# Kernel tuning notes

Measured on AMD Instinct MI355X. Metric: run time of the kernel, lower is better.

## Reference

```python
import jax, jax.numpy as jnp
import numpy as np

D = 256        # in_dim == out_dim for both node types
NH = 8         # n_heads
DH = D // NH   # d_over_h = 32
NA = 50000     # nodes of type 'a'
NB = 20000     # nodes of type 'b'
E = 100000     # edges per edge type
MAX_LEN = 27759
LN_EPS = 1e-5


def _rte_table():
    # Fixed (non-trainable) sinusoidal table from RelativeTemporalEncoding
    pos = np.arange(MAX_LEN, dtype=np.float32)[:, None]
    div = np.exp(np.arange(0, D, 2, dtype=np.float32) * (-np.log(10000.0) / D))
    tab = np.zeros((MAX_LEN, D), dtype=np.float32)
    tab[:, 0::2] = np.sin(pos * div) / np.sqrt(D)
    tab[:, 1::2] = np.cos(pos * div) / np.sqrt(D)
    return jnp.asarray(tab)


def setup_inputs() -> dict:
    key = jax.random.key(0)
    ks = jax.random.split(key, 24)
    s = 1.0 / np.sqrt(D)
    sh = 1.0 / np.sqrt(DH)
    inp = {
        "Ha": jax.random.normal(ks[0], (NA, D), jnp.float32),
        "Hb": jax.random.normal(ks[1], (NB, D), jnp.float32),
        "rte_emb": _rte_table(),
        # stacked per-node-type weights, index 0 -> 'a', 1 -> 'b'; torch Linear layout [out, in]
        "Wq": jax.random.normal(ks[2], (2, D, D), jnp.float32) * s,
        "Wk": jax.random.normal(ks[3], (2, D, D), jnp.float32) * s,
        "Wm": jax.random.normal(ks[4], (2, D, D), jnp.float32) * s,
        "Wa": jax.random.normal(ks[5], (2, D, D), jnp.float32) * s,
        "rteW": jax.random.normal(ks[6], (2, D, D), jnp.float32) * s,
        "rteb": jnp.zeros((2, D), jnp.float32),
        "ln_g": jnp.ones((2, D), jnp.float32),
        "ln_b": jnp.zeros((2, D), jnp.float32),
        "res_alpha": jnp.ones((2,), jnp.float32),
        # stacked per-edge-type params, index 0 -> e1 (a->a), 1 -> e2 (b->a), 2 -> e3 (a->b)
        "Watt": jax.random.normal(ks[7], (3, DH, DH), jnp.float32) * sh,
        "Wmsg": jax.random.normal(ks[8], (3, DH, DH), jnp.float32) * sh,
        "prior": jnp.ones((3,), jnp.float32),
        "src1": jax.random.randint(ks[9], (E,), 0, NA, jnp.int32),
        "dst1": jax.random.randint(ks[10], (E,), 0, NA, jnp.int32),
        "t1": jax.random.randint(ks[11], (E,), 1, MAX_LEN, jnp.int32),
        "src2": jax.random.randint(ks[12], (E,), 0, NB, jnp.int32),
        "dst2": jax.random.randint(ks[13], (E,), 0, NA, jnp.int32),
        "t2": jax.random.randint(ks[14], (E,), 1, MAX_LEN, jnp.int32),
        "src3": jax.random.randint(ks[15], (E,), 0, NA, jnp.int32),
        "dst3": jax.random.randint(ks[16], (E,), 0, NB, jnp.int32),
        "t3": jax.random.randint(ks[17], (E,), 1, MAX_LEN, jnp.int32),
    }
    return inp


def _edge_agg(Hs, Hd, src, dst, t, Wk_s, Wm_s, Wq_t, rW, rb, Wa_e, Wm_e, pr, rte_emb, n_dst):
    """Per-edge-type attention + segment softmax + weighted scatter-sum."""
    ne = src.shape[0]
    # RTE on gathered source features: h_src + Linear(emb[27759 - time])
    hs = Hs[src] + rte_emb[MAX_LEN - t] @ rW.T + rb            # [E, D]
    K = (hs @ Wk_s.T).reshape(ne, NH, DH)                       # [E, H, DH]
    Q = (Hd[dst] @ Wq_t.T).reshape(ne, NH, DH)                  # [E, H, DH]
    att = jnp.einsum('ehd,df,ehf->eh', K, Wa_e, Q) * pr / np.sqrt(DH).astype(np.float32)
    msg = jnp.einsum('ehd,df->ehf', (hs @ Wm_s.T).reshape(ne, NH, DH), Wm_e)
    # segment softmax over destination nodes (DGL mailbox softmax)
    amax = jax.lax.stop_gradient(jax.ops.segment_max(att, dst, num_segments=n_dst))
    ex = jnp.exp(att - amax[dst])
    den = jax.ops.segment_sum(ex, dst, num_segments=n_dst)
    w = ex / den[dst]                                           # [E, H]
    agg = jax.ops.segment_sum(w[..., None] * msg, dst, num_segments=n_dst)  # [N, H, DH]
    cnt = jax.ops.segment_sum(jnp.ones((ne,), jnp.float32), dst, num_segments=n_dst)
    return agg, (cnt > 0).astype(jnp.float32)


def _update(agg, Hx, Wa_n, g, b, ra):
    x = jax.nn.elu(agg.reshape(agg.shape[0], -1)) @ Wa_n.T
    alpha = jax.nn.sigmoid(ra)
    u = alpha * x + (1.0 - alpha) * Hx
    mu = jnp.mean(u, axis=-1, keepdims=True)
    var = jnp.var(u, axis=-1, keepdims=True)
    return (u - mu) / jnp.sqrt(var + LN_EPS) * g + b


def reference(Ha, Hb, rte_emb, Wq, Wk, Wm, Wa, rteW, rteb, ln_g, ln_b, res_alpha,
              Watt, Wmsg, prior, src1, dst1, t1, src2, dst2, t2, src3, dst3, t3):
    # e1: a -> a ; e2: b -> a ; e3: a -> b
    agg1, h1 = _edge_agg(Ha, Ha, src1, dst1, t1, Wk[0], Wm[0], Wq[0], rteW[0], rteb[0], Watt[0], Wmsg[0], prior[0], rte_emb, NA)
    agg2, h2 = _edge_agg(Hb, Ha, src2, dst2, t2, Wk[1], Wm[1], Wq[0], rteW[1], rteb[1], Watt[1], Wmsg[1], prior[1], rte_emb, NA)
    agg3, h3 = _edge_agg(Ha, Hb, src3, dst3, t3, Wk[0], Wm[0], Wq[1], rteW[0], rteb[0], Watt[2], Wmsg[2], prior[2], rte_emb, NB)
    # cross_reducer='mean': average over edge types that delivered messages
    agg_a = (agg1 + agg2) / jnp.maximum(h1 + h2, 1.0)[:, None, None]
    agg_b = agg3 / jnp.maximum(h3, 1.0)[:, None, None]
    out_a = _update(agg_a, Ha, Wa[0], ln_g[0], ln_b[0], res_alpha[0])
    out_b = _update(agg_b, Hb, Wa[1], ln_g[1], ln_b[1], res_alpha[1])
    return (out_a, out_b)
```

## Files before the change

### kernel.cpp

```cpp
#include <hip/hip_runtime.h>
#include <hip/hip_bf16.h>
#include <math.h>

typedef __hip_bfloat16 bf16;
typedef __attribute__((ext_vector_type(8))) short bf16x8v;
typedef __attribute__((ext_vector_type(4))) float f32x4;


__device__ __forceinline__ float eluf(float x) { return x > 0.f ? x : (__expf(x) - 1.f); }
__device__ __forceinline__ float b2f(unsigned short u) { return __uint_as_float((unsigned)u << 16); }
__device__ __forceinline__ unsigned short f2b(float f) {
    unsigned u = __float_as_uint(f);
    return (unsigned short)((u + 0x7fffu + ((u >> 16) & 1u)) >> 16);
}
__device__ __forceinline__ void unpack8(uint4 u, float* o) {
    o[0] = __uint_as_float(u.x << 16); o[1] = __uint_as_float(u.x & 0xffff0000u);
    o[2] = __uint_as_float(u.y << 16); o[3] = __uint_as_float(u.y & 0xffff0000u);
    o[4] = __uint_as_float(u.z << 16); o[5] = __uint_as_float(u.z & 0xffff0000u);
    o[6] = __uint_as_float(u.w << 16); o[7] = __uint_as_float(u.w & 0xffff0000u);
}
__device__ __forceinline__ void unpack4(ushort4 u, float* o) {
    o[0] = b2f(u.x); o[1] = b2f(u.y); o[2] = b2f(u.z); o[3] = b2f(u.w);
}

#define ASYNC_LDS16(g, l) \
    __builtin_amdgcn_global_load_lds((const __attribute__((address_space(1))) void*)(g), \
                                     (__attribute__((address_space(3))) void*)(l), 16, 0, 0)

__global__ void conv_multi_kernel(
    const float* s0, bf16* o0, int n0, const float* s1, bf16* o1, int n1,
    const float* s2, bf16* o2, int n2, const float* s3, bf16* o3, int n3,
    const float* s4, bf16* o4, int n4, const float* s5, bf16* o5, int n5,
    int* z0, int nz0, int* z1, int nz1)
{
    if (blockIdx.y == 6) {
        for (int i = blockIdx.x * 256 + threadIdx.x; i < nz0; i += gridDim.x * 256) z0[i] = 0;
        if (blockIdx.x == 0 && threadIdx.x < (unsigned)nz1) z1[threadIdx.x] = 0;
        return;
    }
    const float* sp; bf16* op; int n8;
    switch (blockIdx.y) {
        case 0: sp = s0; op = o0; n8 = n0; break;
        case 1: sp = s1; op = o1; n8 = n1; break;
        case 2: sp = s2; op = o2; n8 = n2; break;
        case 3: sp = s3; op = o3; n8 = n3; break;
        case 4: sp = s4; op = o4; n8 = n4; break;
        default: sp = s5; op = o5; n8 = n5; break;
    }
    for (int i = blockIdx.x * 256 + threadIdx.x; i < n8; i += gridDim.x * 256) {
        const float4* p = (const float4*)(sp + (size_t)i * 8);
        float4 a = p[0], b = p[1];
        uint4 u;
        u.x = (unsigned)f2b(a.x) | ((unsigned)f2b(a.y) << 16);
        u.y = (unsigned)f2b(a.z) | ((unsigned)f2b(a.w) << 16);
        u.z = (unsigned)f2b(b.x) | ((unsigned)f2b(b.y) << 16);
        u.w = (unsigned)f2b(b.z) | ((unsigned)f2b(b.w) << 16);
        *(uint4*)(op + (size_t)i * 8) = u;
    }
}

__global__ void fold6_kernel(const float* __restrict__ Watt, const float* __restrict__ Wmsg,
                             const float* __restrict__ prior,
                             const float* __restrict__ Wq, const float* __restrict__ Wm,
                             bf16* __restrict__ WcatA, bf16* __restrict__ WcatB,
                             float* __restrict__ Wmx1f, float* __restrict__ Wmx2f,
                             float* __restrict__ Wmx3f)
{
    const int g = blockIdx.x >> 8;
    const int i = blockIdx.x & 255;
    const int j = threadIdx.x;
    const int h = i >> 5, r = i & 31;
    const float* A; const float* W; float sc = 1.f; int tr = 0;
    bf16* ob; float* of = nullptr;
    const float isq = 0.17677669529663687f;
    switch (g) {
        case 0: A = Watt;        sc = prior[0] * isq; W = Wq;         ob = WcatA;                       break;
        case 1: A = Watt + 1024; sc = prior[1] * isq; W = Wq;         ob = WcatA + (size_t)256 * 256;   break;
        case 2: A = Watt + 2048; sc = prior[2] * isq; W = Wq + 65536; ob = WcatB;                       break;
        case 3: A = Wmsg;        tr = 1; W = Wm;         ob = WcatA + (size_t)768 * 256;  of = Wmx1f;   break;
        case 4: A = Wmsg + 1024; tr = 1; W = Wm + 65536; ob = WcatB + (size_t)512 * 256;  of = Wmx2f;   break;
        default:A = Wmsg + 2048; tr = 1; W = Wm;         ob = WcatA + (size_t)1024 * 256; of = Wmx3f;   break;
    }
    __shared__ float arow[32];
    if (j < 32) arow[j] = (tr ? A[j * 32 + r] : A[r * 32 + j]) * sc;
    __syncthreads();
    float acc = 0.f;
    for (int k = 0; k < 32; ++k) acc += arow[k] * W[(size_t)(h * 32 + k) * 256 + j];
    ((unsigned short*)ob)[(size_t)i * 256 + j] = f2b(acc);
    if (of) of[(size_t)i * 256 + j] = acc;
}

__global__ void combine5_kernel(const float* __restrict__ Wk,
                                const float* __restrict__ Wmx1f, const float* __restrict__ Wmx2f,
                                const float* __restrict__ Wmx3f,
                                const float* __restrict__ rteW, const float* __restrict__ rteb,
                                bf16* __restrict__ WcatR, float* __restrict__ bcatR)
{
    const int g = blockIdx.x >> 8;
    const int i = blockIdx.x & 255;
    const int j = threadIdx.x;
    const float* Wp; const float* rW; const float* rb; int op;
    switch (g) {
        case 0: Wp = Wk;         rW = rteW;         rb = rteb;       op = 0; break;
        case 1: Wp = Wk + 65536; rW = rteW + 65536; rb = rteb + 256; op = 2; break;
        case 2: Wp = Wmx1f;      rW = rteW;         rb = rteb;       op = 1; break;
        case 3: Wp = Wmx2f;      rW = rteW + 65536; rb = rteb + 256; op = 3; break;
        default:Wp = Wmx3f;      rW = rteW;         rb = rteb;       op = 4; break;
    }
    __shared__ float wrow[256];
    wrow[j] = Wp[i * 256 + j];
    __syncthreads();
    float acc = 0.f;
    for (int k = 0; k < 256; ++k) acc += wrow[k] * rW[k * 256 + j];
    ((unsigned short*)WcatR)[(size_t)(op * 256 + i) * 256 + j] = f2b(acc);
    if (j == 0) {
        float b = 0.f;
        for (int k = 0; k < 256; ++k) b += wrow[k] * rb[k];
        bcatR[op * 256 + i] = b;
    }
}

__device__ __forceinline__ void gemm_body(
    const bf16* __restrict__ A, const bf16* __restrict__ Wcat,
    const float* __restrict__ bcat,
    bf16* C0, bf16* C1, bf16* C2, bf16* C3, bf16* C4,
    int wideMask, int M, int bx, int by, char* As, char* Bs)
{
    const int tid = threadIdx.x;
    const int wid = tid >> 6, lane = tid & 63;
    const size_t row0 = (size_t)bx * 128;
    const int gcol0 = by * 128;
    const int cb = by >> 1;
    const int lcol0 = (by & 1) * 128;
    bf16* Csel = (cb == 0) ? C0 : (cb == 1) ? C1 : (cb == 2) ? C2 : (cb == 3) ? C3 : C4;
    const size_t cstride = ((wideMask >> cb) & 1) ? 512 : 256;
    const int wr = wid >> 1, wc = wid & 1;

    f32x4 zero = {0.f, 0.f, 0.f, 0.f};
    f32x4 acc[4][4];
#pragma unroll
    for (int m = 0; m < 4; ++m)
#pragma unroll
        for (int n = 0; n < 4; ++n) acc[m][n] = zero;

    const int sr = wid * 32 + (lane >> 3);
    const int scc = (lane & 7) << 4;
    const char* Ab = (const char*)A;
    const char* Wb = (const char*)Wcat;

    for (int k0 = 0; k0 < 512; k0 += 128) {
#pragma unroll
        for (int i = 0; i < 4; ++i) {
            const int r = sr + i * 8;
            const int csw = scc ^ ((r & 7) << 4);
            const int ldso = wid * 4096 + i * 1024;
            ASYNC_LDS16(Ab + (row0 + r) * 512 + k0 + csw, As + ldso);
            ASYNC_LDS16(Wb + (size_t)(gcol0 + r) * 512 + k0 + csw, Bs + ldso);
        }
        __syncthreads();
#pragma unroll
        for (int kk = 0; kk < 2; ++kk) {
            bf16x8v a[4], b[4];
            const int cbase = kk * 64 + ((lane >> 4) << 4);
#pragma unroll
            for (int m = 0; m < 4; ++m) {
                const int r = wr * 64 + m * 16 + (lane & 15);
                a[m] = *(const bf16x8v*)(As + r * 128 + (cbase ^ ((r & 7) << 4)));
            }
#pragma unroll
            for (int n = 0; n < 4; ++n) {
                const int r = wc * 64 + n * 16 + (lane & 15);
                b[n] = *(const bf16x8v*)(Bs + r * 128 + (cbase ^ ((r & 7) << 4)));
            }
#pragma unroll
            for (int m = 0; m < 4; ++m)
#pragma unroll
                for (int n = 0; n < 4; ++n)
                    acc[m][n] = __builtin_amdgcn_mfma_f32_16x16x32_bf16(a[m], b[n], acc[m][n], 0, 0, 0);
        }
        __syncthreads();
    }
    const int orow = (lane >> 4) << 2;
    const int ocol = lane & 15;
    float bv[4];
#pragma unroll
    for (int n = 0; n < 4; ++n)
        bv[n] = bcat ? bcat[gcol0 + wc * 64 + n * 16 + ocol] : 0.f;
    unsigned short* Cp = (unsigned short*)Csel;
#pragma unroll
    for (int m = 0; m < 4; ++m) {
#pragma unroll
        for (int j = 0; j < 4; ++j) {
            const size_t row = row0 + wr * 64 + m * 16 + orow + j;
            if ((int)row >= M) continue;
#pragma unroll
            for (int n = 0; n < 4; ++n) {
                const int col = lcol0 + wc * 64 + n * 16 + ocol;
                Cp[row * cstride + col] = f2b(acc[m][n][j] + bv[n]);
            }
        }
    }
}

__global__ __launch_bounds__(256) void gemm3_kernel(
    const bf16* A0, const bf16* W0, const float* bc0,
    bf16* o00, bf16* o01, bf16* o02, bf16* o03, bf16* o04, int mask0, int M0,
    const bf16* A1, const bf16* W1,
    bf16* o10, bf16* o11, bf16* o12, bf16* o13, bf16* o14, int mask1, int M1,
    const bf16* A2, const bf16* W2,
    bf16* o20, bf16* o21, bf16* o22, int mask2, int M2,
    int b0, int b1)
{
    __shared__ __align__(16) char As[16384];
    __shared__ __align__(16) char Bs[16384];
    const int bid = blockIdx.x;
    if (bid < b0) {
        gemm_body(A0, W0, bc0, o00, o01, o02, o03, o04, mask0, M0,
                  bid / 10, bid % 10, As, Bs);
    } else if (bid < b1) {
        const int lid = bid - b0;
        gemm_body(A1, W1, nullptr, o10, o11, o12, o13, o14, mask1, M1,
                  lid / 10, lid % 10, As, Bs);
    } else {
        const int lid = bid - b1;
        gemm_body(A2, W2, nullptr, o20, o21, o22, o22, o22, mask2, M2,
                  lid / 6, lid % 6, As, Bs);
    }
}

__global__ __launch_bounds__(512) void ugemm_ln_kernel(
    const bf16* __restrict__ AG, const bf16* __restrict__ Wp,
    const bf16* __restrict__ Hbf, const float* __restrict__ g,
    const float* __restrict__ b, const float* __restrict__ ra,
    float* __restrict__ out, int M)
{
    __shared__ __align__(16) char As[16384];
    __shared__ __align__(16) char Bs[32768];
    __shared__ float red[128][8];
    const int tid = threadIdx.x;
    const int wid = tid >> 6, lane = tid & 63;
    const int wr = wid >> 2, wc = wid & 3;
    const size_t row0 = (size_t)blockIdx.x * 128;

    f32x4 zero = {0.f, 0.f, 0.f, 0.f};
    f32x4 acc[4][4];
#pragma unroll
    for (int m = 0; m < 4; ++m)
#pragma unroll
        for (int n = 0; n < 4; ++n) acc[m][n] = zero;

    const char* Ab = (const char*)AG;
    const char* Wb = (const char*)Wp;
    for (int k0 = 0; k0 < 512; k0 += 128) {
#pragma unroll
        for (int i = 0; i < 2; ++i) {
            const int r = wid * 16 + i * 8 + (lane >> 3);
            const int csw = ((lane & 7) << 4) ^ ((r & 7) << 4);
            ASYNC_LDS16(Ab + (row0 + r) * 512 + k0 + csw, As + (wid * 16 + i * 8) * 128);
        }
#pragma unroll
        for (int i = 0; i < 4; ++i) {
            const int r = wid * 32 + i * 8 + (lane >> 3);
            const int csw = ((lane & 7) << 4) ^ ((r & 7) << 4);
            ASYNC_LDS16(Wb + (size_t)r * 512 + k0 + csw, Bs + (wid * 32 + i * 8) * 128);
        }
        __syncthreads();
#pragma unroll
        for (int kk = 0; kk < 2; ++kk) {
            bf16x8v a[4], bv[4];
            const int cbase = kk * 64 + ((lane >> 4) << 4);
#pragma unroll
            for (int m = 0; m < 4; ++m) {
                const int r = wr * 64 + m * 16 + (lane & 15);
                a[m] = *(const bf16x8v*)(As + r * 128 + (cbase ^ ((r & 7) << 4)));
            }
#pragma unroll
            for (int n = 0; n < 4; ++n) {
                const int r = wc * 64 + n * 16 + (lane & 15);
                bv[n] = *(const bf16x8v*)(Bs + r * 128 + (cbase ^ ((r & 7) << 4)));
            }
#pragma unroll
            for (int m = 0; m < 4; ++m)
#pragma unroll
                for (int n = 0; n < 4; ++n)
                    acc[m][n] = __builtin_amdgcn_mfma_f32_16x16x32_bf16(a[m], bv[n], acc[m][n], 0, 0, 0);
        }
        __syncthreads();
    }
    const float alpha = 1.f / (1.f + __expf(-ra[0]));
    const float beta = 1.f - alpha;
    const int orow = (lane >> 4) << 2;
    const int ocol = lane & 15;
    float gv[4], bb[4];
#pragma unroll
    for (int n = 0; n < 4; ++n) {
        gv[n] = g[wc * 64 + n * 16 + ocol];
        bb[n] = b[wc * 64 + n * 16 + ocol];
    }
    const unsigned short* Hp = (const unsigned short*)Hbf;
#pragma unroll
    for (int m = 0; m < 4; ++m) {
#pragma unroll
        for (int j = 0; j < 4; ++j) {
            const int rl = wr * 64 + m * 16 + orow + j;
            const size_t grow = row0 + rl;
            float s = 0.f, s2 = 0.f;
#pragma unroll
            for (int n = 0; n < 4; ++n) {
                const int col = wc * 64 + n * 16 + ocol;
                float hv = ((int)grow < M) ? b2f(Hp[grow * 256 + col]) : 0.f;
                float u = alpha * acc[m][n][j] + beta * hv;
                acc[m][n][j] = u;
                s += u; s2 += u * u;
            }
            s += __shfl_xor(s, 1); s2 += __shfl_xor(s2, 1);
            s += __shfl_xor(s, 2); s2 += __shfl_xor(s2, 2);
            s += __shfl_xor(s, 4); s2 += __shfl_xor(s2, 4);
            s += __shfl_xor(s, 8); s2 += __shfl_xor(s2, 8);
            if (ocol == 0) { red[rl][wc] = s; red[rl][4 + wc] = s2; }
        }
    }
    __syncthreads();
#pragma unroll
    for (int m = 0; m < 4; ++m) {
#pragma unroll
        for (int j = 0; j < 4; ++j) {
            const int rl = wr * 64 + m * 16 + orow + j;
            const size_t grow = row0 + rl;
            if ((int)grow >= M) continue;
            float S = red[rl][0] + red[rl][1] + red[rl][2] + red[rl][3];
            float S2 = red[rl][4] + red[rl][5] + red[rl][6] + red[rl][7];
            const float mu = S * 0.00390625f;
            const float var = S2 * 0.00390625f - mu * mu;
            const float inv = rsqrtf(var + 1e-5f);
#pragma unroll
            for (int n = 0; n < 4; ++n) {
                const int col = wc * 64 + n * 16 + ocol;
                out[grow * 256 + col] = (acc[m][n][j] - mu) * inv * gv[n] + bb[n];
            }
        }
    }
}

__global__ void hist3_kernel(const int* __restrict__ d1, const int* __restrict__ d2,
                             const int* __restrict__ d3, int* __restrict__ c1,
                             int* __restrict__ c2, int* __restrict__ c3,
                             int E1, int E2, int E3)
{
    int i = blockIdx.x * 256 + threadIdx.x;
    if (i < E1) atomicAdd(&c1[d1[i]], 1);
    else if (i < E1 + E2) atomicAdd(&c2[d2[i - E1]], 1);
    else if (i < E1 + E2 + E3) atomicAdd(&c3[d3[i - E1 - E2]], 1);
}
__global__ void alloc3b_kernel(const int* __restrict__ cnt, int* __restrict__ start,
                               int* __restrict__ cursor, int* __restrict__ gtot,
                               int NA, int NB)
{
    const int slot = blockIdx.y;
    const int base = (slot == 0) ? 0 : (slot == 1) ? NA : 2 * NA;
    const int len = (slot == 2) ? NB : NA;
    int i = blockIdx.x * 256 + threadIdx.x;
    if (i >= len) return;
    int* gp = gtot + slot;
    int idx = base + i;
    int s = atomicAdd(gp, cnt[idx]);
    start[idx] = s; cursor[idx] = s;
}
__global__ void scatter3_kernel(const int* __restrict__ d1, const int* __restrict__ d2,
                                const int* __restrict__ d3, int* __restrict__ cur1,
                                int* __restrict__ cur2, int* __restrict__ cur3,
                                int* __restrict__ el1, int* __restrict__ el2,
                                int* __restrict__ el3, int E1, int E2, int E3)
{
    int i = blockIdx.x * 256 + threadIdx.x;
    if (i < E1) { int p = atomicAdd(&cur1[d1[i]], 1); el1[p] = i; }
    else if (i < E1 + E2) { int e = i - E1; int p = atomicAdd(&cur2[d2[e]], 1); el2[p] = e; }
    else if (i < E1 + E2 + E3) { int e = i - E1 - E2; int p = atomicAdd(&cur3[d3[e]], 1); el3[p] = e; }
}

__device__ __forceinline__ void epass16(
    const bf16* __restrict__ KM, const bf16* __restrict__ RKM,
    const int* __restrict__ srcv, const int* __restrict__ tv, const int* __restrict__ el,
    int beg, int num, const float q[8], int ml, int lane, int srcl,
    float s[8], float& denOut)
{
    float den = 0.f;
    for (int c0 = 0; c0 < num; c0 += 64) {
        int nc = num - c0; if (nc > 64) nc = 64;
        int sx_l = 0, tt_l = 0;
        if (lane < nc) { int e = el[beg + c0 + lane]; sx_l = srcv[e]; tt_l = ml - tv[e]; }
        int sx = __shfl(sx_l, 0), tt = __shfl(tt_l, 0);
        uint4 km = *(const uint4*)(KM + (size_t)sx * 512 + lane * 8);
        uint4 rm = *(const uint4*)(RKM + (size_t)tt * 512 + lane * 8);
        for (int i = 0; i < nc; ++i) {
            uint4 kmn = km, rmn = rm;
            if (i + 1 < nc) {
                int sxn = __shfl(sx_l, i + 1), ttn = __shfl(tt_l, i + 1);
                kmn = *(const uint4*)(KM + (size_t)sxn * 512 + lane * 8);
                rmn = *(const uint4*)(RKM + (size_t)ttn * 512 + lane * 8);
            }
            float a[8], b[8];
            unpack8(km, a); unpack8(rm, b);
#pragma unroll
            for (int x = 0; x < 8; ++x) a[x] += b[x];
            float p = a[0] * q[0] + a[1] * q[1] + a[2] * q[2] + a[3] * q[3]
                    + a[4] * q[4] + a[5] * q[5] + a[6] * q[6] + a[7] * q[7];
            p += __shfl_xor(p, 1); p += __shfl_xor(p, 2);
            float ex = __expf(p);
            float exb = __shfl(ex, srcl);
            den += exb;
#pragma unroll
            for (int x = 0; x < 8; ++x) s[x] += exb * a[x];
            km = kmn; rm = rmn;
        }
    }
    denOut = den;
}

__device__ __forceinline__ void epass8(
    const bf16* __restrict__ Kh, const bf16* __restrict__ RKh,
    const bf16* __restrict__ Mt, const bf16* __restrict__ RMt,
    const int* __restrict__ srcv, const int* __restrict__ tv, const int* __restrict__ el,
    int beg, int num, const float q[4], int ml, int lane,
    float s[4], float& denOut)
{
    float den = 0.f;
    for (int c0 = 0; c0 < num; c0 += 64) {
        int nc = num - c0; if (nc > 64) nc = 64;
        int sx_l = 0, tt_l = 0;
        if (lane < nc) { int e = el[beg + c0 + lane]; sx_l = srcv[e]; tt_l = ml - tv[e]; }
        int sx = __shfl(sx_l, 0), tt = __shfl(tt_l, 0);
        ushort4 kv = *(const ushort4*)(Kh + (size_t)sx * 512 + lane * 4);
        ushort4 rv = *(const ushort4*)(RKh + (size_t)tt * 512 + lane * 4);
        ushort4 mv = *(const ushort4*)(Mt + (size_t)sx * 256 + lane * 4);
        ushort4 uv = *(const ushort4*)(RMt + (size_t)tt * 256 + lane * 4);
        for (int i = 0; i < nc; ++i) {
            ushort4 kn = kv, rn = rv, mn = mv, un = uv;
            if (i + 1 < nc) {
                int sxn = __shfl(sx_l, i + 1), ttn = __shfl(tt_l, i + 1);
                kn = *(const ushort4*)(Kh + (size_t)sxn * 512 + lane * 4);
                rn = *(const ushort4*)(RKh + (size_t)ttn * 512 + lane * 4);
                mn = *(const ushort4*)(Mt + (size_t)sxn * 256 + lane * 4);
                un = *(const ushort4*)(RMt + (size_t)ttn * 256 + lane * 4);
            }
            float a[4], b[4], m[4], r[4];
            unpack4(kv, a); unpack4(rv, b); unpack4(mv, m); unpack4(uv, r);
            float p = (a[0] + b[0]) * q[0] + (a[1] + b[1]) * q[1]
                    + (a[2] + b[2]) * q[2] + (a[3] + b[3]) * q[3];
            p += __shfl_xor(p, 1); p += __shfl_xor(p, 2); p += __shfl_xor(p, 4);
            float ex = __expf(p);
            den += ex;
#pragma unroll
            for (int x = 0; x < 4; ++x) s[x] += ex * (m[x] + r[x]);
            kv = kn; rv = rn; mv = mn; uv = un;
        }
    }
    denOut = den;
}

__global__ __launch_bounds__(256) void edge_fused_kernel(
    const bf16* __restrict__ Qa1, const bf16* __restrict__ Qa2,
    const bf16* __restrict__ KMa1, const bf16* __restrict__ RKM1,
    const int* __restrict__ src1, const int* __restrict__ t1,
    const int* __restrict__ start1, const int* __restrict__ cnt1, const int* __restrict__ el1,
    const bf16* __restrict__ KMb, const bf16* __restrict__ RKM2,
    const int* __restrict__ src2, const int* __restrict__ t2,
    const int* __restrict__ start2, const int* __restrict__ cnt2, const int* __restrict__ el2,
    bf16* __restrict__ AGa, int NA,
    const bf16* __restrict__ Qb3, const bf16* __restrict__ Ma3, const bf16* __restrict__ RM3p,
    const int* __restrict__ src3, const int* __restrict__ t3,
    const int* __restrict__ start3, const int* __restrict__ cnt3, const int* __restrict__ el3,
    bf16* __restrict__ AGb, int NB, int ml, int nablk)
{
    const int wid = threadIdx.x >> 6, lane = threadIdx.x & 63;
    if ((int)blockIdx.x < nablk) {
        const int n = blockIdx.x * 4 + wid;
        if (n >= NA) return;
        float q1[8], q2[8];
        unpack8(*(const uint4*)(Qa1 + (size_t)n * 256 + (lane & 31) * 8), q1);
        unpack8(*(const uint4*)(Qa2 + (size_t)n * 256 + (lane & 31) * 8), q2);
        const int srcl = (lane < 32) ? lane : (((lane - 32) >> 2) << 2);
        const int num1 = cnt1[n], num2 = cnt2[n];
        float sf[8] = {0.f, 0.f, 0.f, 0.f, 0.f, 0.f, 0.f, 0.f};
        float s[8], den;
        if (num1 > 0) {
#pragma unroll
            for (int x = 0; x < 8; ++x) s[x] = 0.f;
            epass16(KMa1, RKM1, src1, t1, el1, start1[n], num1, q1, ml, lane, srcl, s, den);
            float invd = 1.f / den;
#pragma unroll
            for (int x = 0; x < 8; ++x) sf[x] += s[x] * invd;
        }
        if (num2 > 0) {
#pragma unroll
            for (int x = 0; x < 8; ++x) s[x] = 0.f;
            epass16(KMb, RKM2, src2, t2, el2, start2[n], num2, q2, ml, lane, srcl, s, den);
            float invd = 1.f / den;
#pragma unroll
            for (int x = 0; x < 8; ++x) sf[x] += s[x] * invd;
        }
        float dv = 1.f / fmaxf((float)((num1 > 0) + (num2 > 0)), 1.f);
        if (lane >= 32) {
            uint4 o;
            o.x = (unsigned)f2b(eluf(sf[0] * dv)) | ((unsigned)f2b(eluf(sf[1] * dv)) << 16);
            o.y = (unsigned)f2b(eluf(sf[2] * dv)) | ((unsigned)f2b(eluf(sf[3] * dv)) << 16);
            o.z = (unsigned)f2b(eluf(sf[4] * dv)) | ((unsigned)f2b(eluf(sf[5] * dv)) << 16);
            o.w = (unsigned)f2b(eluf(sf[6] * dv)) | ((unsigned)f2b(eluf(sf[7] * dv)) << 16);
            *(uint4*)((unsigned short*)AGa + (size_t)n * 256 + (lane - 32) * 8) = o;
        }
    } else {
        const int n = ((int)blockIdx.x - nablk) * 4 + wid;
        if (n >= NB) return;
        float q3[4];
        unpack4(*(const ushort4*)(Qb3 + (size_t)n * 256 + lane * 4), q3);
        const int num3 = cnt3[n];
        float s[4] = {0.f, 0.f, 0.f, 0.f};
        float den = 1.f;
        if (num3 > 0) {
            epass8(KMa1, RKM1, Ma3, RM3p, src3, t3, el3, start3[n], num3, q3, ml, lane, s, den);
            float invd = 1.f / den;
#pragma unroll
            for (int x = 0; x < 4; ++x) s[x] *= invd;
        }
        ushort4 o;
        o.x = f2b(eluf(s[0])); o.y = f2b(eluf(s[1]));
        o.z = f2b(eluf(s[2])); o.w = f2b(eluf(s[3]));
        *(ushort4*)((unsigned short*)AGb + (size_t)n * 256 + lane * 4) = o;
    }
}

extern "C" void kernel_launch(void* const* d_in, const int* in_sizes, int n_in,
                              void* d_out, int out_size, void* d_ws, size_t ws_size,
                              hipStream_t stream)
{
    const float* Ha   = (const float*)d_in[0];
    const float* Hb   = (const float*)d_in[1];
    const float* rte  = (const float*)d_in[2];
    const float* Wq   = (const float*)d_in[3];
    const float* Wk   = (const float*)d_in[4];
    const float* Wm   = (const float*)d_in[5];
    const float* Wa   = (const float*)d_in[6];
    const float* rteW = (const float*)d_in[7];
    const float* rteb = (const float*)d_in[8];
    const float* ln_g = (const float*)d_in[9];
    const float* ln_b = (const float*)d_in[10];
    const float* ra   = (const float*)d_in[11];
    const float* Watt = (const float*)d_in[12];
    const float* Wmsg = (const float*)d_in[13];
    const float* prior= (const float*)d_in[14];
    const int* src1 = (const int*)d_in[15];
    const int* dst1 = (const int*)d_in[16];
    const int* t1   = (const int*)d_in[17];
    const int* src2 = (const int*)d_in[18];
    const int* dst2 = (const int*)d_in[19];
    const int* t2   = (const int*)d_in[20];
    const int* src3 = (const int*)d_in[21];
    const int* dst3 = (const int*)d_in[22];
    const int* t3   = (const int*)d_in[23];

    const int NA = in_sizes[0] / 256;
    const int NB = in_sizes[1] / 256;
    const int ML = in_sizes[2] / 256;
    const int E1 = in_sizes[15];
    const int E2 = in_sizes[18];
    const int E3 = in_sizes[21];
    const int NAp = (NA + 127) & ~127;
    const int NBp = (NB + 127) & ~127;
    const int MLp = (ML + 127) & ~127;

    char* w = (char*)d_ws;
    size_t off = 0;
    auto alloc = [&](size_t bytes) -> void* {
        void* p = w + off;
        off += (bytes + 511) & ~(size_t)511;
        return p;
    };
    bf16* WcatA = (bf16*)alloc((size_t)1280 * 256 * 2);
    bf16* WcatB = (bf16*)alloc((size_t)768 * 256 * 2);
    bf16* WcatR = (bf16*)alloc((size_t)1280 * 256 * 2);
    float* bcatR = (float*)alloc(1280 * 4);
    bf16* Wa_bf = (bf16*)alloc(131072 * 2);
    float* Wmx1f = (float*)alloc(65536 * 4);
    float* Wmx2f = (float*)alloc(65536 * 4);
    float* Wmx3f = (float*)alloc(65536 * 4);
    bf16* Ha_bf = (bf16*)alloc((size_t)NAp * 512);
    bf16* Hb_bf = (bf16*)alloc((size_t)NBp * 512);
    bf16* rte_bf = (bf16*)alloc((size_t)MLp * 512);
    bf16* Qa1 = (bf16*)alloc((size_t)NAp * 512);
    bf16* Qa2 = (bf16*)alloc((size_t)NAp * 512);
    bf16* KMa1 = (bf16*)alloc((size_t)NAp * 1024);
    bf16* RKM1 = (bf16*)alloc((size_t)MLp * 1024);
    bf16* RKM2 = (bf16*)alloc((size_t)MLp * 1024);
    bf16* RM3p = (bf16*)alloc((size_t)MLp * 512);
    int* cnt = (int*)alloc((size_t)(NA + NA + NB) * 4);
    int* cnt1 = cnt, *cnt2 = cnt + NA, *cnt3 = cnt + 2 * NA;
    int* startb = (int*)alloc((size_t)(NA + NA + NB) * 4);
    int* start1 = startb, *start2 = startb + NA, *start3 = startb + 2 * NA;
    int* curb = (int*)alloc((size_t)(NA + NA + NB) * 4);
    int* cur1 = curb, *cur2 = curb + NA, *cur3 = curb + 2 * NA;
    int* elist1 = (int*)alloc((size_t)E1 * 4);
    int* elist2 = (int*)alloc((size_t)E2 * 4);
    int* elist3 = (int*)alloc((size_t)E3 * 4);
    int* gtot = (int*)alloc(16);
    bf16* Ma3 = (bf16*)d_out;
    bf16* Qb3 = (bf16*)d_out + (size_t)NAp * 256;
    bf16* KMb = (bf16*)d_out + (size_t)NAp * 256 + (size_t)NBp * 256;
    bf16* AGa = Qa1;
    bf16* AGb = Qb3;

    conv_multi_kernel<<<dim3(512, 7), 256, 0, stream>>>(
        Ha, Ha_bf, NA * 32, Hb, Hb_bf, NB * 32, rte, rte_bf, ML * 32,
        Wa, Wa_bf, 16384,
        Wk, WcatA + (size_t)512 * 256, 8192,
        Wk + 65536, WcatB + (size_t)256 * 256, 8192,
        cnt, NA + NA + NB, gtot, 4);
    fold6_kernel<<<1536, 256, 0, stream>>>(Watt, Wmsg, prior, Wq, Wm,
                                           WcatA, WcatB, Wmx1f, Wmx2f, Wmx3f);
    combine5_kernel<<<1280, 256, 0, stream>>>(Wk, Wmx1f, Wmx2f, Wmx3f, rteW, rteb, WcatR, bcatR);

    int Etot = E1 + E2 + E3;
    hist3_kernel<<<dim3((Etot + 255) / 256), 256, 0, stream>>>(dst1, dst2, dst3, cnt1, cnt2, cnt3, E1, E2, E3);
    alloc3b_kernel<<<dim3((NA + 255) / 256, 3), 256, 0, stream>>>(cnt, startb, curb, gtot, NA, NB);
    scatter3_kernel<<<dim3((Etot + 255) / 256), 256, 0, stream>>>(
        dst1, dst2, dst3, cur1, cur2, cur3, elist1, elist2, elist3, E1, E2, E3);

    const int nx0 = MLp / 128, nx1 = NAp / 128, nx2 = NBp / 128;
    const int b0 = nx0 * 10;
    const int b1 = b0 + nx1 * 10;
    const int btot = b1 + nx2 * 6;
    gemm3_kernel<<<dim3(btot), 256, 0, stream>>>(
        rte_bf, WcatR, bcatR, RKM1, RKM1 + 256, RKM2, RKM2 + 256, RM3p, 0xF, ML,
        Ha_bf, WcatA, Qa1, Qa2, KMa1, KMa1 + 256, Ma3, 0xC, NA,
        Hb_bf, WcatB, Qb3, KMb, KMb + 256, 0x6, NB,
        b0, b1);

    const int nablk = (NA + 3) / 4;
    const int nbblk = (NB + 3) / 4;
    edge_fused_kernel<<<dim3(nablk + nbblk), 256, 0, stream>>>(
        Qa1, Qa2, KMa1, RKM1, src1, t1, start1, cnt1, elist1,
        KMb, RKM2, src2, t2, start2, cnt2, elist2,
        AGa, NA,
        Qb3, Ma3, RM3p, src3, t3, start3, cnt3, elist3,
        AGb, NB, ML, nablk);

    float* out = (float*)d_out;
    ugemm_ln_kernel<<<dim3(NBp / 128), 512, 0, stream>>>(
        AGb, Wa_bf + 65536, Hb_bf, ln_g + 256, ln_b + 256, ra + 1,
        out + (size_t)NA * 256, NB);
    ugemm_ln_kernel<<<dim3(NAp / 128), 512, 0, stream>>>(
        AGa, Wa_bf, Ha_bf, ln_g, ln_b, ra, out, NA);
}
```

Measured before the change: 380.7 us.

## Pack src/time into CSR edge list and batch gathers four edges at a time

The scatter kernel now writes (src, ml - t) pairs straight into the CSR edge list, so the edge kernel no longer does a dependent double indirection through el then src/t. The per-edge gather loop is unrolled to issue four edges' K/M row loads before computing, which gives more memory-level parallelism than one-ahead prefetch. First-chunk edge indices are loaded up front for both edge types, and the Q2 unpack is deferred until needed. The cost is doubled edge-list storage and more registers held by the four-way unrolled loads, which may reduce occupancy.

```diff
diff --git a/kernel.cpp b/kernel.cpp
--- a/kernel.cpp
+++ b/kernel.cpp
@@ -367,51 +367,84 @@
     start[idx] = s; cursor[idx] = s;
 }
 __global__ void scatter3_kernel(const int* __restrict__ d1, const int* __restrict__ d2,
-                                const int* __restrict__ d3, int* __restrict__ cur1,
-                                int* __restrict__ cur2, int* __restrict__ cur3,
-                                int* __restrict__ el1, int* __restrict__ el2,
-                                int* __restrict__ el3, int E1, int E2, int E3)
+                                const int* __restrict__ d3,
+                                const int* __restrict__ s1, const int* __restrict__ s2,
+                                const int* __restrict__ s3,
+                                const int* __restrict__ tv1, const int* __restrict__ tv2,
+                                const int* __restrict__ tv3,
+                                int* __restrict__ cur1, int* __restrict__ cur2,
+                                int* __restrict__ cur3,
+                                int2* __restrict__ el1, int2* __restrict__ el2,
+                                int2* __restrict__ el3, int E1, int E2, int E3, int ml)
 {
     int i = blockIdx.x * 256 + threadIdx.x;
-    if (i < E1) { int p = atomicAdd(&cur1[d1[i]], 1); el1[p] = i; }
-    else if (i < E1 + E2) { int e = i - E1; int p = atomicAdd(&cur2[d2[e]], 1); el2[p] = e; }
-    else if (i < E1 + E2 + E3) { int e = i - E1 - E2; int p = atomicAdd(&cur3[d3[e]], 1); el3[p] = e; }
+    if (i < E1) {
+        int p = atomicAdd(&cur1[d1[i]], 1);
+        el1[p] = make_int2(s1[i], ml - tv1[i]);
+    } else if (i < E1 + E2) {
+        int e = i - E1; int p = atomicAdd(&cur2[d2[e]], 1);
+        el2[p] = make_int2(s2[e], ml - tv2[e]);
+    } else if (i < E1 + E2 + E3) {
+        int e = i - E1 - E2; int p = atomicAdd(&cur3[d3[e]], 1);
+        el3[p] = make_int2(s3[e], ml - tv3[e]);
+    }
 }
 
 __device__ __forceinline__ void epass16(
     const bf16* __restrict__ KM, const bf16* __restrict__ RKM,
-    const int* __restrict__ srcv, const int* __restrict__ tv, const int* __restrict__ el,
-    int beg, int num, const float q[8], int ml, int lane, int srcl,
+    const int2* __restrict__ el, int beg, int num,
+    int sx_l, int tt_l,
+    const float q[8], int lane, int srcl,
     float s[8], float& denOut)
 {
     float den = 0.f;
+    const char* KMb = (const char*)KM + lane * 16;
+    const char* RMb = (const char*)RKM + lane * 16;
+    auto edge = [&](uint4 km, uint4 rm) {
+        float a[8], b[8];
+        unpack8(km, a); unpack8(rm, b);
+#pragma unroll
+        for (int x = 0; x < 8; ++x) a[x] += b[x];
+        float p = a[0] * q[0] + a[1] * q[1] + a[2] * q[2] + a[3] * q[3]
+                + a[4] * q[4] + a[5] * q[5] + a[6] * q[6] + a[7] * q[7];
+        p += __shfl_xor(p, 1); p += __shfl_xor(p, 2);
+        float ex = __expf(p);
+        float exb = __shfl(ex, srcl);
+        den += exb;
+#pragma unroll
+        for (int x = 0; x < 8; ++x) s[x] += exb * a[x];
+    };
     for (int c0 = 0; c0 < num; c0 += 64) {
         int nc = num - c0; if (nc > 64) nc = 64;
-        int sx_l = 0, tt_l = 0;
-        if (lane < nc) { int e = el[beg + c0 + lane]; sx_l = srcv[e]; tt_l = ml - tv[e]; }
-        int sx = __shfl(sx_l, 0), tt = __shfl(tt_l, 0);
-        uint4 km = *(const uint4*)(KM + (size_t)sx * 512 + lane * 8);
-        uint4 rm = *(const uint4*)(RKM + (size_t)tt * 512 + lane * 8);
-        for (int i = 0; i < nc; ++i) {
-            uint4 kmn = km, rmn = rm;
-            if (i + 1 < nc) {
-                int sxn = __shfl(sx_l, i + 1), ttn = __shfl(tt_l, i + 1);
-                kmn = *(const uint4*)(KM + (size_t)sxn * 512 + lane * 8);
-                rmn = *(const uint4*)(RKM + (size_t)ttn * 512 + lane * 8);
-            }
-            float a[8], b[8];
-            unpack8(km, a); unpack8(rm, b);
-#pragma unroll
-            for (int x = 0; x < 8; ++x) a[x] += b[x];
-            float p = a[0] * q[0] + a[1] * q[1] + a[2] * q[2] + a[3] * q[3]
-                    + a[4] * q[4] + a[5] * q[5] + a[6] * q[6] + a[7] * q[7];
-            p += __shfl_xor(p, 1); p += __shfl_xor(p, 2);
-            float ex = __expf(p);
-            float exb = __shfl(ex, srcl);
-            den += exb;
-#pragma unroll
-            for (int x = 0; x < 8; ++x) s[x] += exb * a[x];
-            km = kmn; rm = rmn;
+        if (c0 > 0) {
+            sx_l = 0; tt_l = 0;
+            if (lane < nc) { int2 e = el[beg + c0 + lane]; sx_l = e.x; tt_l = e.y; }
+        }
+        for (int i0 = 0; i0 < nc; i0 += 4) {
+            const int rem = nc - i0;
+            const int a0 = __shfl(sx_l, i0),     b0 = __shfl(tt_l, i0);
+            const int a1 = __shfl(sx_l, i0 | 1), b1 = __shfl(tt_l, i0 | 1);
+            const int a2 = __shfl(sx_l, i0 | 2), b2 = __shfl(tt_l, i0 | 2);
+            const int a3 = __shfl(sx_l, i0 | 3), b3 = __shfl(tt_l, i0 | 3);
+            uint4 km0, rm0, km1, rm1, km2, rm2, km3, rm3;
+            km0 = *(const uint4*)(KMb + (size_t)a0 * 1024);
+            rm0 = *(const uint4*)(RMb + (size_t)b0 * 1024);
+            if (rem > 1) {
+                km1 = *(const uint4*)(KMb + (size_t)a1 * 1024);
+                rm1 = *(const uint4*)(RMb + (size_t)b1 * 1024);
+            }
+            if (rem > 2) {
+                km2 = *(const uint4*)(KMb + (size_t)a2 * 1024);
+                rm2 = *(const uint4*)(RMb + (size_t)b2 * 1024);
+            }
+            if (rem > 3) {
+                km3 = *(const uint4*)(KMb + (size_t)a3 * 1024);
+                rm3 = *(const uint4*)(RMb + (size_t)b3 * 1024);
+            }
+            edge(km0, rm0);
+            if (rem > 1) edge(km1, rm1);
+            if (rem > 2) edge(km2, rm2);
+            if (rem > 3) edge(km3, rm3);
         }
     }
     denOut = den;
@@ -420,39 +453,66 @@
 __device__ __forceinline__ void epass8(
     const bf16* __restrict__ Kh, const bf16* __restrict__ RKh,
     const bf16* __restrict__ Mt, const bf16* __restrict__ RMt,
-    const int* __restrict__ srcv, const int* __restrict__ tv, const int* __restrict__ el,
-    int beg, int num, const float q[4], int ml, int lane,
+    const int2* __restrict__ el, int beg, int num,
+    int sx_l, int tt_l,
+    const float q[4], int lane,
     float s[4], float& denOut)
 {
     float den = 0.f;
+    const char* Kb = (const char*)Kh + lane * 8;
+    const char* Rb = (const char*)RKh + lane * 8;
+    const char* Mb = (const char*)Mt + lane * 8;
+    const char* Ub = (const char*)RMt + lane * 8;
+    auto edge = [&](ushort4 kv, ushort4 rv, ushort4 mv, ushort4 uv) {
+        float a[4], b[4], m[4], r[4];
+        unpack4(kv, a); unpack4(rv, b); unpack4(mv, m); unpack4(uv, r);
+        float p = (a[0] + b[0]) * q[0] + (a[1] + b[1]) * q[1]
+                + (a[2] + b[2]) * q[2] + (a[3] + b[3]) * q[3];
+        p += __shfl_xor(p, 1); p += __shfl_xor(p, 2); p += __shfl_xor(p, 4);
+        float ex = __expf(p);
+        den += ex;
+#pragma unroll
+        for (int x = 0; x < 4; ++x) s[x] += ex * (m[x] + r[x]);
+    };
     for (int c0 = 0; c0 < num; c0 += 64) {
         int nc = num - c0; if (nc > 64) nc = 64;
-        int sx_l = 0, tt_l = 0;
-        if (lane < nc) { int e = el[beg + c0 + lane]; sx_l = srcv[e]; tt_l = ml - tv[e]; }
-        int sx = __shfl(sx_l, 0), tt = __shfl(tt_l, 0);
-        ushort4 kv = *(const ushort4*)(Kh + (size_t)sx * 512 + lane * 4);
-        ushort4 rv = *(const ushort4*)(RKh + (size_t)tt * 512 + lane * 4);
-        ushort4 mv = *(const ushort4*)(Mt + (size_t)sx * 256 + lane * 4);
-        ushort4 uv = *(const ushort4*)(RMt + (size_t)tt * 256 + lane * 4);
-        for (int i = 0; i < nc; ++i) {
-            ushort4 kn = kv, rn = rv, mn = mv, un = uv;
-            if (i + 1 < nc) {
-                int sxn = __shfl(sx_l, i + 1), ttn = __shfl(tt_l, i + 1);
-                kn = *(const ushort4*)(Kh + (size_t)sxn * 512 + lane * 4);
-                rn = *(const ushort4*)(RKh + (size_t)ttn * 512 + lane * 4);
-                mn = *(const ushort4*)(Mt + (size_t)sxn * 256 + lane * 4);
-                un = *(const ushort4*)(RMt + (size_t)ttn * 256 + lane * 4);
-            }
-            float a[4], b[4], m[4], r[4];
-            unpack4(kv, a); unpack4(rv, b); unpack4(mv, m); unpack4(uv, r);
-            float p = (a[0] + b[0]) * q[0] + (a[1] + b[1]) * q[1]
-                    + (a[2] + b[2]) * q[2] + (a[3] + b[3]) * q[3];
-            p += __shfl_xor(p, 1); p += __shfl_xor(p, 2); p += __shfl_xor(p, 4);
-            float ex = __expf(p);
-            den += ex;
-#pragma unroll
-            for (int x = 0; x < 4; ++x) s[x] += ex * (m[x] + r[x]);
-            kv = kn; rv = rn; mv = mn; uv = un;
+        if (c0 > 0) {
+            sx_l = 0; tt_l = 0;
+            if (lane < nc) { int2 e = el[beg + c0 + lane]; sx_l = e.x; tt_l = e.y; }
+        }
+        for (int i0 = 0; i0 < nc; i0 += 4) {
+            const int rem = nc - i0;
+            const int a0 = __shfl(sx_l, i0),     b0 = __shfl(tt_l, i0);
+            const int a1 = __shfl(sx_l, i0 | 1), b1 = __shfl(tt_l, i0 | 1);
+            const int a2 = __shfl(sx_l, i0 | 2), b2 = __shfl(tt_l, i0 | 2);
+            const int a3 = __shfl(sx_l, i0 | 3), b3 = __shfl(tt_l, i0 | 3);
+            ushort4 k0, r0, m0, u0, k1, r1, m1, u1, k2, r2, m2, u2, k3, r3, m3, u3;
+            k0 = *(const ushort4*)(Kb + (size_t)a0 * 1024);
+            r0 = *(const ushort4*)(Rb + (size_t)b0 * 1024);
+            m0 = *(const ushort4*)(Mb + (size_t)a0 * 512);
+            u0 = *(const ushort4*)(Ub + (size_t)b0 * 512);
+            if (rem > 1) {
+                k1 = *(const ushort4*)(Kb + (size_t)a1 * 1024);
+                r1 = *(const ushort4*)(Rb + (size_t)b1 * 1024);
+                m1 = *(const ushort4*)(Mb + (size_t)a1 * 512);
+                u1 = *(const ushort4*)(Ub + (size_t)b1 * 512);
+            }
+            if (rem > 2) {
+                k2 = *(const ushort4*)(Kb + (size_t)a2 * 1024);
+                r2 = *(const ushort4*)(Rb + (size_t)b2 * 1024);
+                m2 = *(const ushort4*)(Mb + (size_t)a2 * 512);
+                u2 = *(const ushort4*)(Ub + (size_t)b2 * 512);
+            }
+            if (rem > 3) {
+                k3 = *(const ushort4*)(Kb + (size_t)a3 * 1024);
+                r3 = *(const ushort4*)(Rb + (size_t)b3 * 1024);
+                m3 = *(const ushort4*)(Mb + (size_t)a3 * 512);
+                u3 = *(const ushort4*)(Ub + (size_t)b3 * 512);
+            }
+            edge(k0, r0, m0, u0);
+            if (rem > 1) edge(k1, r1, m1, u1);
+            if (rem > 2) edge(k2, r2, m2, u2);
+            if (rem > 3) edge(k3, r3, m3, u3);
         }
     }
     denOut = den;
@@ -461,40 +521,43 @@
 __global__ __launch_bounds__(256) void edge_fused_kernel(
     const bf16* __restrict__ Qa1, const bf16* __restrict__ Qa2,
     const bf16* __restrict__ KMa1, const bf16* __restrict__ RKM1,
-    const int* __restrict__ src1, const int* __restrict__ t1,
-    const int* __restrict__ start1, const int* __restrict__ cnt1, const int* __restrict__ el1,
+    const int* __restrict__ start1, const int* __restrict__ cnt1, const int2* __restrict__ el1,
     const bf16* __restrict__ KMb, const bf16* __restrict__ RKM2,
-    const int* __restrict__ src2, const int* __restrict__ t2,
-    const int* __restrict__ start2, const int* __restrict__ cnt2, const int* __restrict__ el2,
+    const int* __restrict__ start2, const int* __restrict__ cnt2, const int2* __restrict__ el2,
     bf16* __restrict__ AGa, int NA,
     const bf16* __restrict__ Qb3, const bf16* __restrict__ Ma3, const bf16* __restrict__ RM3p,
-    const int* __restrict__ src3, const int* __restrict__ t3,
-    const int* __restrict__ start3, const int* __restrict__ cnt3, const int* __restrict__ el3,
-    bf16* __restrict__ AGb, int NB, int ml, int nablk)
+    const int* __restrict__ start3, const int* __restrict__ cnt3, const int2* __restrict__ el3,
+    bf16* __restrict__ AGb, int NB, int nablk)
 {
     const int wid = threadIdx.x >> 6, lane = threadIdx.x & 63;
     if ((int)blockIdx.x < nablk) {
         const int n = blockIdx.x * 4 + wid;
         if (n >= NA) return;
-        float q1[8], q2[8];
+        const int num1 = cnt1[n], num2 = cnt2[n];
+        const int beg1 = start1[n], beg2 = start2[n];
+        int sx1 = 0, tt1 = 0, sx2 = 0, tt2 = 0;
+        if (lane < (num1 < 64 ? num1 : 64)) { int2 e = el1[beg1 + lane]; sx1 = e.x; tt1 = e.y; }
+        if (lane < (num2 < 64 ? num2 : 64)) { int2 e = el2[beg2 + lane]; sx2 = e.x; tt2 = e.y; }
+        float q1[8];
         unpack8(*(const uint4*)(Qa1 + (size_t)n * 256 + (lane & 31) * 8), q1);
-        unpack8(*(const uint4*)(Qa2 + (size_t)n * 256 + (lane & 31) * 8), q2);
+        const uint4 qv2 = *(const uint4*)(Qa2 + (size_t)n * 256 + (lane & 31) * 8);
         const int srcl = (lane < 32) ? lane : (((lane - 32) >> 2) << 2);
-        const int num1 = cnt1[n], num2 = cnt2[n];
         float sf[8] = {0.f, 0.f, 0.f, 0.f, 0.f, 0.f, 0.f, 0.f};
         float s[8], den;
         if (num1 > 0) {
 #pragma unroll
             for (int x = 0; x < 8; ++x) s[x] = 0.f;
-            epass16(KMa1, RKM1, src1, t1, el1, start1[n], num1, q1, ml, lane, srcl, s, den);
+            epass16(KMa1, RKM1, el1, beg1, num1, sx1, tt1, q1, lane, srcl, s, den);
             float invd = 1.f / den;
 #pragma unroll
             for (int x = 0; x < 8; ++x) sf[x] += s[x] * invd;
         }
         if (num2 > 0) {
+            float q2[8];
+            unpack8(qv2, q2);
 #pragma unroll
             for (int x = 0; x < 8; ++x) s[x] = 0.f;
-            epass16(KMb, RKM2, src2, t2, el2, start2[n], num2, q2, ml, lane, srcl, s, den);
+            epass16(KMb, RKM2, el2, beg2, num2, sx2, tt2, q2, lane, srcl, s, den);
             float invd = 1.f / den;
 #pragma unroll
             for (int x = 0; x < 8; ++x) sf[x] += s[x] * invd;
@@ -511,13 +574,16 @@
     } else {
         const int n = ((int)blockIdx.x - nablk) * 4 + wid;
         if (n >= NB) return;
+        const int num3 = cnt3[n];
+        const int beg3 = start3[n];
+        int sx3 = 0, tt3 = 0;
+        if (lane < (num3 < 64 ? num3 : 64)) { int2 e = el3[beg3 + lane]; sx3 = e.x; tt3 = e.y; }
         float q3[4];
         unpack4(*(const ushort4*)(Qb3 + (size_t)n * 256 + lane * 4), q3);
-        const int num3 = cnt3[n];
         float s[4] = {0.f, 0.f, 0.f, 0.f};
         float den = 1.f;
         if (num3 > 0) {
-            epass8(KMa1, RKM1, Ma3, RM3p, src3, t3, el3, start3[n], num3, q3, ml, lane, s, den);
+            epass8(KMa1, RKM1, Ma3, RM3p, el3, beg3, num3, sx3, tt3, q3, lane, s, den);
             float invd = 1.f / den;
 #pragma unroll
             for (int x = 0; x < 4; ++x) s[x] *= invd;
@@ -598,9 +664,9 @@
     int* start1 = startb, *start2 = startb + NA, *start3 = startb + 2 * NA;
     int* curb = (int*)alloc((size_t)(NA + NA + NB) * 4);
     int* cur1 = curb, *cur2 = curb + NA, *cur3 = curb + 2 * NA;
-    int* elist1 = (int*)alloc((size_t)E1 * 4);
-    int* elist2 = (int*)alloc((size_t)E2 * 4);
-    int* elist3 = (int*)alloc((size_t)E3 * 4);
+    int2* elist1 = (int2*)alloc((size_t)E1 * 8);
+    int2* elist2 = (int2*)alloc((size_t)E2 * 8);
+    int2* elist3 = (int2*)alloc((size_t)E3 * 8);
     int* gtot = (int*)alloc(16);
     bf16* Ma3 = (bf16*)d_out;
     bf16* Qb3 = (bf16*)d_out + (size_t)NAp * 256;
@@ -622,7 +688,8 @@
     hist3_kernel<<<dim3((Etot + 255) / 256), 256, 0, stream>>>(dst1, dst2, dst3, cnt1, cnt2, cnt3, E1, E2, E3);
     alloc3b_kernel<<<dim3((NA + 255) / 256, 3), 256, 0, stream>>>(cnt, startb, curb, gtot, NA, NB);
     scatter3_kernel<<<dim3((Etot + 255) / 256), 256, 0, stream>>>(
-        dst1, dst2, dst3, cur1, cur2, cur3, elist1, elist2, elist3, E1, E2, E3);
+        dst1, dst2, dst3, src1, src2, src3, t1, t2, t3,
+        cur1, cur2, cur3, elist1, elist2, elist3, E1, E2, E3, ML);
 
     const int nx0 = MLp / 128, nx1 = NAp / 128, nx2 = NBp / 128;
     const int b0 = nx0 * 10;
@@ -637,11 +704,11 @@
     const int nablk = (NA + 3) / 4;
     const int nbblk = (NB + 3) / 4;
     edge_fused_kernel<<<dim3(nablk + nbblk), 256, 0, stream>>>(
-        Qa1, Qa2, KMa1, RKM1, src1, t1, start1, cnt1, elist1,
-        KMb, RKM2, src2, t2, start2, cnt2, elist2,
+        Qa1, Qa2, KMa1, RKM1, start1, cnt1, elist1,
+        KMb, RKM2, start2, cnt2, elist2,
         AGa, NA,
-        Qb3, Ma3, RM3p, src3, t3, start3, cnt3, elist3,
-        AGb, NB, ML, nablk);
+        Qb3, Ma3, RM3p, start3, cnt3, elist3,
+        AGb, NB, nablk);
 
     float* out = (float*)d_out;
     ugemm_ln_kernel<<<dim3(NBp / 128), 512, 0, stream>>>(
```

Result: no change. 373.9 us (-1.8%).
